# Kernel tuning notes

Hardware: AMD Instinct MI355X
Metric: run time of the kernel (lower is better)

## Reference

```python
import jax, jax.numpy as jnp
import numpy as np

L = 4          # dilation_depth
HID = 32       # hidden_channels
F_IN = 16
F_OUT = 16
K = 2          # conv kernel size


def setup_inputs() -> dict:
    key = jax.random.key(0)
    ks = jax.random.split(key, 20)
    B, T, N, F = 8, 512, 128, F_IN
    s = 0.1
    inp = {
        "X": jax.random.normal(ks[0], (B, T, N, F), jnp.float32),
        "A": jax.random.normal(ks[1], (N, N), jnp.float32) / jnp.sqrt(N).astype(jnp.float32),
        "in_w": jax.random.normal(ks[2], (F, 3 * HID), jnp.float32) * s,
        "in_b": jnp.zeros((3 * HID,), jnp.float32),
        "ct_w": jax.random.normal(ks[3], (L, K, HID, HID), jnp.float32) * s,
        "ct_b": jnp.zeros((L, HID), jnp.float32),
        "cs_w": jax.random.normal(ks[4], (L, K, HID, HID), jnp.float32) * s,
        "cs_b": jnp.zeros((L, HID), jnp.float32),
        "gcn_w": jax.random.normal(ks[5], (L, HID, HID), jnp.float32) * s,
        "gcn_b": jnp.zeros((L, HID), jnp.float32),
        "res_w": jax.random.normal(ks[6], (L, HID, HID), jnp.float32) * s,
        "res_b": jnp.zeros((L, HID), jnp.float32),
        "skip_w": jax.random.normal(ks[7], (L, HID, HID), jnp.float32) * s,
        "skip_b": jnp.zeros((L, HID), jnp.float32),
        "out1_w": jax.random.normal(ks[8], (HID, HID), jnp.float32) * s,
        "out1_b": jnp.zeros((HID,), jnp.float32),
        "out2_w": jax.random.normal(ks[9], (HID, F_OUT), jnp.float32) * s,
        "out2_b": jnp.zeros((F_OUT,), jnp.float32),
    }
    return inp


def _causal_conv(x, w, b, dilation):
    # x: [BN, T, C]; w: [K, C_in, C_out] (WIO); causal pad left by dilation*(K-1)
    pad = dilation * (w.shape[0] - 1)
    y = jax.lax.conv_general_dilated(
        x, w, window_strides=(1,), padding=[(pad, 0)],
        rhs_dilation=(dilation,), dimension_numbers=("NWC", "WIO", "NWC"))
    return y + b


def reference(X, A, in_w, in_b, ct_w, ct_b, cs_w, cs_b, gcn_w, gcn_b,
              res_w, res_b, skip_w, skip_b, out1_w, out1_b, out2_w, out2_b):
    B, T, N, F = X.shape
    Xp = X @ in_w + in_b                      # [B,T,N,3H]
    x_a, x_b, x_res = jnp.split(Xp, 3, axis=-1)
    H = x_a.shape[-1]
    # Faithful to source: raw reshape [B,T,N,H] -> [B*N,T,H] (no transpose), as in the original code.
    x_a_r = x_a.reshape(B * N, T, H)
    x_b_r = x_b.reshape(B * N, T, H)
    skip = jnp.zeros_like(x_res)
    for i in range(L):
        d = 2 ** i
        tcn = (jnp.tanh(_causal_conv(x_a_r, ct_w[i], ct_b[i], d))
               * jax.nn.sigmoid(_causal_conv(x_b_r, cs_w[i], cs_b[i], d)))
        tcn = tcn.reshape(B, N, T, H).transpose(0, 2, 1, 3)   # [B,T,N,H]
        gcn = jnp.einsum('ij,btjf->btif', A, x_res) @ gcn_w[i] + gcn_b[i]
        h = tcn + gcn
        x_res = (h @ res_w[i] + res_b[i]) + x_res
        skip = skip + (h @ skip_w[i] + skip_b[i])
    h = jax.nn.relu(skip)
    h = jax.nn.relu(h @ out1_w + out1_b)
    return h @ out2_w + out2_b
```

## Files before the change

kernel.cpp:

```cpp
#include <hip/hip_runtime.h>
#include <math.h>

#define T_ 512

typedef _Float16 half8 __attribute__((ext_vector_type(8)));
typedef _Float16 half4 __attribute__((ext_vector_type(4)));
typedef float f32x4 __attribute__((ext_vector_type(4)));

__device__ __forceinline__ float ts_act(float a, float b) {
    float e2a = __expf(a + a);
    float eb  = __expf(b);
    float num = (e2a - 1.0f) * eb;
    float den = (e2a + 1.0f) * (eb + 1.0f);
    return num * __builtin_amdgcn_rcpf(den);
}

__device__ __forceinline__ half4 pack4(f32x4 v) {
    half4 h;
    h[0] = (_Float16)v[0]; h[1] = (_Float16)v[1];
    h[2] = (_Float16)v[2]; h[3] = (_Float16)v[3];
    return h;
}

__global__ __launch_bounds__(256) void k_prep(
    const float* __restrict__ A,     const float* __restrict__ in_w,
    const float* __restrict__ in_b,
    const float* __restrict__ ct_w,  const float* __restrict__ ct_b,
    const float* __restrict__ cs_w,  const float* __restrict__ cs_b,
    const float* __restrict__ gcn_w, const float* __restrict__ res_w,
    const float* __restrict__ skip_w,
    const float* __restrict__ out1_w,const float* __restrict__ out2_w,
    _Float16* __restrict__ FR, float* __restrict__ BIAS)
{
    int idx = blockIdx.x * 256 + threadIdx.x;
    if (idx < 16384) {
        int j = idx & 7, L = (idx >> 3) & 63, tile = idx >> 9;
        int it = tile >> 2, kt = tile & 3;
        FR[idx] = (_Float16)A[(it * 16 + (L & 15)) * 128 + kt * 32 + (L >> 4) * 8 + j];
    } else if (idx < 24576) {
        int e = idx - 16384;
        int j = e & 7, L = (e >> 3) & 63, ct = (e >> 9) & 1, mat = e >> 10;
        int k = (L >> 4) * 8 + j, col = ct * 16 + (L & 15);
        int l = mat >> 1, br = mat & 1;
        const float* tw = (br ? cs_w : ct_w) + l * 2048;
        int bro = br * 32;
        float v = 0.f;
        if (k < 16) { for (int c = 0; c < 32; ++c) v += in_w[k*96 + bro + c] * tw[c*32 + col]; }
        else        { for (int c = 0; c < 32; ++c) v += in_w[(k-16)*96 + bro + c] * tw[1024 + c*32 + col]; }
        FR[idx] = (_Float16)v;
    } else if (idx < 39936) {
        int e = idx - 24576;
        int i = e & 3, L = (e >> 2) & 63, ct = (e >> 8) & 1, ks = (e >> 9) & 1, mat = e >> 10;
        int k = ks * 16 + (L >> 4) * 4 + i, col = ct * 16 + (L & 15);
        float v;
        if (mat < 12) {
            int l = mat / 3, r = mat - l * 3;
            const float* W = (r == 0) ? gcn_w : (r == 1) ? res_w : skip_w;
            v = W[l * 1024 + k * 32 + col];
        } else if (mat == 12) v = out1_w[k * 32 + col];
        else if (mat == 13)   v = (ct == 0) ? out2_w[k * 16 + (L & 15)] : 0.f;
        else                  v = (ks == 0) ? in_w[k * 96 + 64 + col] : 0.f;
        FR[idx] = (_Float16)v;
    } else if (idx < 40448) {
        int e = idx - 39936;
        int n = e & 31, br = (e >> 5) & 1, pvi = (e >> 6) & 1, l = e >> 7;
        const float* W  = br ? cs_w : ct_w;
        const float* bb = br ? cs_b : ct_b;
        int ibo = br * 32;
        float v = bb[l * 32 + n];
        for (int c = 0; c < 32; ++c) v += in_b[ibo + c] * W[l*2048 + 1024 + c*32 + n];
        if (pvi)
            for (int c = 0; c < 32; ++c) v += in_b[ibo + c] * W[l*2048 + c*32 + n];
        BIAS[e] = v;
    }
}

__global__ __launch_bounds__(256, 3) void k_fused(
    const float* __restrict__ X,
    const _Float16* __restrict__ FR,
    const float* __restrict__ BIAS,
    const float* __restrict__ in_b,
    const float* __restrict__ gcn_b,
    const float* __restrict__ res_b,
    const float* __restrict__ skip_b,
    const float* __restrict__ b1,
    const float* __restrict__ b2,
    float* __restrict__ out)
{
    __shared__ _Float16 Pld[128 * 88];
    __shared__ _Float16 xsT[2][32 * 136];

    const int bx = blockIdx.x;
    const int btid = ((bx & 7) << 9) | (bx >> 3);
    const int b = btid >> 9, t = btid & (T_ - 1);
    const int tid = threadIdx.x, lane = tid & 63, w = tid >> 6;
    const int lm = lane & 15, kb = lane >> 4;
    const int R = w * 32;
    const int row = lane >> 1, ch = lane & 1;

    const half8* AFv  = (const half8*)FR;
    const half8* W32v = (const half8*)(FR + 16384);
    const half4* W16v = (const half4*)(FR + 24576);
    const f32x4 zero4 = {0.f, 0.f, 0.f, 0.f};

    {
        const size_t nrow = (size_t)(b * 128 + R + row) * T_;
        const float4* xc = (const float4*)(X + (nrow + t) * 16 + ch * 8);
        float4 c0 = xc[0], c1 = xc[1];
        float4 p0[4], p1[4];
#pragma unroll
        for (int l = 0; l < 4; ++l) {
            const int d = 1 << l;
            if (t >= d) {
                const float4* xp = (const float4*)(X + (nrow + (t - d)) * 16 + ch * 8);
                p0[l] = xp[0]; p1[l] = xp[1];
            } else {
                p0[l] = make_float4(0.f, 0.f, 0.f, 0.f);
                p1[l] = make_float4(0.f, 0.f, 0.f, 0.f);
            }
        }
        half8 hv;
        hv[0]=(_Float16)c0.x; hv[1]=(_Float16)c0.y; hv[2]=(_Float16)c0.z; hv[3]=(_Float16)c0.w;
        hv[4]=(_Float16)c1.x; hv[5]=(_Float16)c1.y; hv[6]=(_Float16)c1.z; hv[7]=(_Float16)c1.w;
        *(half8*)&Pld[(R + row) * 88 + 64 + ch * 8] = hv;
#pragma unroll
        for (int l = 0; l < 4; ++l) {
            hv[0]=(_Float16)p0[l].x; hv[1]=(_Float16)p0[l].y; hv[2]=(_Float16)p0[l].z; hv[3]=(_Float16)p0[l].w;
            hv[4]=(_Float16)p1[l].x; hv[5]=(_Float16)p1[l].y; hv[6]=(_Float16)p1[l].z; hv[7]=(_Float16)p1[l].w;
            *(half8*)&Pld[(R + row) * 88 + l * 16 + ch * 8] = hv;
        }
    }

    f32x4 xm[2][2], skT[2][2];
    {
        const float4 x0 = *(const float4*)(X + ((size_t)btid * 128 + R + lm) * 16 + kb * 4);
        const float4 x1 = *(const float4*)(X + ((size_t)btid * 128 + R + 16 + lm) * 16 + kb * 4);
        half4 p0, p1;
        p0[0]=(_Float16)x0.x; p0[1]=(_Float16)x0.y; p0[2]=(_Float16)x0.z; p0[3]=(_Float16)x0.w;
        p1[0]=(_Float16)x1.x; p1[1]=(_Float16)x1.y; p1[2]=(_Float16)x1.z; p1[3]=(_Float16)x1.w;
#pragma unroll
        for (int f = 0; f < 2; ++f) {
            half4 wi = W16v[(56 + f) * 64 + lane];
            float bi = in_b[64 + f * 16 + lm];
            f32x4 cb; cb[0] = bi; cb[1] = bi; cb[2] = bi; cb[3] = bi;
            xm[0][f] = __builtin_amdgcn_mfma_f32_16x16x16f16(p0, wi, cb, 0, 0, 0);
            xm[1][f] = __builtin_amdgcn_mfma_f32_16x16x16f16(p1, wi, cb, 0, 0, 0);
        }
#pragma unroll
        for (int f3 = 0; f3 < 2; ++f3) {
            f32x4 s = zero4;
#pragma unroll
            for (int l = 0; l < 4; ++l) {
                const float4 q = *(const float4*)&skip_b[l * 32 + f3 * 16 + kb * 4];
                s[0] += q.x; s[1] += q.y; s[2] += q.z; s[3] += q.w;
            }
            skT[f3][0] = s; skT[f3][1] = s;
        }
    }

    const int fragoff = (kb < 2) ? kb * 8 : 64 + (kb - 2) * 8;
    const int lstep   = (kb < 2) ? 16 : 0;

#pragma unroll 1
    for (int l = 0; l < 4; ++l) {
        const bool pv = (t >= (1 << l));
        const float* B2 = BIAS + (l * 2 + (pv ? 1 : 0)) * 64;
        const int buf = l & 1;

#pragma unroll
        for (int mt = 0; mt < 2; ++mt)
#pragma unroll
            for (int f = 0; f < 2; ++f)
                *(half4*)&xsT[buf][(f * 16 + lm) * 136 + R + mt * 16 + kb * 4] = pack4(xm[mt][f]);

        half8 Afr[2][4];
#pragma unroll
        for (int mt = 0; mt < 2; ++mt)
#pragma unroll
            for (int kt = 0; kt < 4; ++kt)
                Afr[mt][kt] = AFv[((w * 2 + mt) * 4 + kt) * 64 + lane];
        const f32x4 cT0 = *(const f32x4*)&B2[0 * 16 + kb * 4];
        const f32x4 cT1 = *(const f32x4*)&B2[1 * 16 + kb * 4];
        const f32x4 cS0 = *(const f32x4*)&B2[32 + 0 * 16 + kb * 4];
        const f32x4 cS1 = *(const f32x4*)&B2[32 + 1 * 16 + kb * 4];

        __syncthreads();

        const int poff = fragoff + l * lstep;
        half8 pf0 = *(const half8*)&Pld[(R + lm) * 88 + poff];
        half8 pf1 = *(const half8*)&Pld[(R + 16 + lm) * 88 + poff];
        f32x4 dt[2][2], ds[2][2];
#pragma unroll
        for (int ct = 0; ct < 2; ++ct) {
            half8 wt = W32v[((l * 2 + 0) * 2 + ct) * 64 + lane];
            half8 ws = W32v[((l * 2 + 1) * 2 + ct) * 64 + lane];
            const f32x4 cT = ct ? cT1 : cT0;
            const f32x4 cS = ct ? cS1 : cS0;
            dt[ct][0] = __builtin_amdgcn_mfma_f32_16x16x32_f16(wt, pf0, cT, 0, 0, 0);
            dt[ct][1] = __builtin_amdgcn_mfma_f32_16x16x32_f16(wt, pf1, cT, 0, 0, 0);
            ds[ct][0] = __builtin_amdgcn_mfma_f32_16x16x32_f16(ws, pf0, cS, 0, 0, 0);
            ds[ct][1] = __builtin_amdgcn_mfma_f32_16x16x32_f16(ws, pf1, cS, 0, 0, 0);
        }

        f32x4 AxT[2][2];
#pragma unroll
        for (int f = 0; f < 2; ++f) {
            half8 xa[4];
#pragma unroll
            for (int kt = 0; kt < 4; ++kt)
                xa[kt] = *(const half8*)&xsT[buf][(f * 16 + lm) * 136 + kt * 32 + kb * 8];
#pragma unroll
            for (int mt = 0; mt < 2; ++mt) {
                f32x4 acc = zero4;
#pragma unroll
                for (int kt = 0; kt < 4; ++kt)
                    acc = __builtin_amdgcn_mfma_f32_16x16x32_f16(xa[kt], Afr[mt][kt], acc, 0, 0, 0);
                AxT[f][mt] = acc;
            }
        }

        f32x4 tcv[2][2];
#pragma unroll
        for (int ct = 0; ct < 2; ++ct)
#pragma unroll
            for (int mt = 0; mt < 2; ++mt)
#pragma unroll
                for (int r = 0; r < 4; ++r)
                    tcv[ct][mt][r] = ts_act(dt[ct][mt][r], ds[ct][mt][r]);

        half4 axh[2][2];
#pragma unroll
        for (int f = 0; f < 2; ++f)
#pragma unroll
            for (int mt = 0; mt < 2; ++mt) axh[f][mt] = pack4(AxT[f][mt]);
        half4 hh[2][2];
#pragma unroll
        for (int g = 0; g < 2; ++g) {
            half4 gw0 = W16v[((l * 3 + 0) * 4 + 0 + g) * 64 + lane];
            half4 gw1 = W16v[((l * 3 + 0) * 4 + 2 + g) * 64 + lane];
            const f32x4 gq = *(const f32x4*)&gcn_b[l * 32 + g * 16 + kb * 4];
#pragma unroll
            for (int mt = 0; mt < 2; ++mt) {
                f32x4 acc = __builtin_amdgcn_mfma_f32_16x16x16f16(gw0, axh[0][mt], gq, 0, 0, 0);
                acc = __builtin_amdgcn_mfma_f32_16x16x16f16(gw1, axh[1][mt], acc, 0, 0, 0);
#pragma unroll
                for (int r = 0; r < 4; ++r) acc[r] += tcv[g][mt][r];
                hh[g][mt] = pack4(acc);
            }
        }

#pragma unroll
        for (int mt = 0; mt < 2; ++mt)
#pragma unroll
            for (int f3 = 0; f3 < 2; ++f3) {
                half4 rw0 = W16v[((l * 3 + 1) * 4 + 0 + f3) * 64 + lane];
                half4 rw1 = W16v[((l * 3 + 1) * 4 + 2 + f3) * 64 + lane];
                f32x4 acc = __builtin_amdgcn_mfma_f32_16x16x16f16(hh[0][mt], rw0, xm[mt][f3], 0, 0, 0);
                xm[mt][f3] = __builtin_amdgcn_mfma_f32_16x16x16f16(hh[1][mt], rw1, acc, 0, 0, 0);
                float rb = res_b[l * 32 + f3 * 16 + lm];
#pragma unroll
                for (int r = 0; r < 4; ++r) xm[mt][f3][r] += rb;

                half4 sw0 = W16v[((l * 3 + 2) * 4 + 0 + f3) * 64 + lane];
                half4 sw1 = W16v[((l * 3 + 2) * 4 + 2 + f3) * 64 + lane];
                f32x4 acs = __builtin_amdgcn_mfma_f32_16x16x16f16(sw0, hh[0][mt], skT[f3][mt], 0, 0, 0);
                skT[f3][mt] = __builtin_amdgcn_mfma_f32_16x16x16f16(sw1, hh[1][mt], acs, 0, 0, 0);
            }
    }

    half4 rs[2][2];
#pragma unroll
    for (int g = 0; g < 2; ++g)
#pragma unroll
        for (int mt = 0; mt < 2; ++mt) {
            f32x4 v;
#pragma unroll
            for (int r = 0; r < 4; ++r) v[r] = fmaxf(skT[g][mt][r], 0.f);
            rs[g][mt] = pack4(v);
        }
    half4 h1h[2][2];
#pragma unroll
    for (int g4 = 0; g4 < 2; ++g4) {
        half4 w10 = W16v[(48 + 0 + g4) * 64 + lane];
        half4 w11 = W16v[(48 + 2 + g4) * 64 + lane];
        const f32x4 bq = *(const f32x4*)&b1[g4 * 16 + kb * 4];
#pragma unroll
        for (int mt = 0; mt < 2; ++mt) {
            f32x4 acc = __builtin_amdgcn_mfma_f32_16x16x16f16(w10, rs[0][mt], bq, 0, 0, 0);
            acc = __builtin_amdgcn_mfma_f32_16x16x16f16(w11, rs[1][mt], acc, 0, 0, 0);
            f32x4 v;
#pragma unroll
            for (int r = 0; r < 4; ++r) v[r] = fmaxf(acc[r], 0.f);
            h1h[g4][mt] = pack4(v);
        }
    }
    {
        half4 w20 = W16v[(52 + 0) * 64 + lane];
        half4 w21 = W16v[(52 + 2) * 64 + lane];
        const f32x4 b2q = *(const f32x4*)&b2[kb * 4];
#pragma unroll
        for (int mt = 0; mt < 2; ++mt) {
            f32x4 acc = __builtin_amdgcn_mfma_f32_16x16x16f16(w20, h1h[0][mt], b2q, 0, 0, 0);
            acc = __builtin_amdgcn_mfma_f32_16x16x16f16(w21, h1h[1][mt], acc, 0, 0, 0);
            float4 o = make_float4(acc[0], acc[1], acc[2], acc[3]);
            *(float4*)&out[((size_t)btid * 128 + R + mt * 16 + lm) * 16 + kb * 4] = o;
        }
    }
}

extern "C" void kernel_launch(void* const* d_in, const int* in_sizes, int n_in,
                              void* d_out, int out_size, void* d_ws, size_t ws_size,
                              hipStream_t stream)
{
    const float* X      = (const float*)d_in[0];
    const float* A      = (const float*)d_in[1];
    const float* in_w   = (const float*)d_in[2];
    const float* in_b   = (const float*)d_in[3];
    const float* ct_w   = (const float*)d_in[4];
    const float* ct_b   = (const float*)d_in[5];
    const float* cs_w   = (const float*)d_in[6];
    const float* cs_b   = (const float*)d_in[7];
    const float* gcn_w  = (const float*)d_in[8];
    const float* gcn_b  = (const float*)d_in[9];
    const float* res_w  = (const float*)d_in[10];
    const float* res_b  = (const float*)d_in[11];
    const float* skip_w = (const float*)d_in[12];
    const float* skip_b = (const float*)d_in[13];
    const float* out1_w = (const float*)d_in[14];
    const float* out1_b = (const float*)d_in[15];
    const float* out2_w = (const float*)d_in[16];
    const float* out2_b = (const float*)d_in[17];

    _Float16* FR   = (_Float16*)d_ws;
    float*    BIAS = (float*)((char*)d_ws + 79872);

    k_prep<<<158, 256, 0, stream>>>(A, in_w, in_b, ct_w, ct_b, cs_w, cs_b,
                                    gcn_w, res_w, skip_w, out1_w, out2_w,
                                    FR, BIAS);

    k_fused<<<8 * T_, 256, 0, stream>>>(X, FR, BIAS, in_b,
                                        gcn_b, res_b, skip_b,
                                        out1_b, out2_b, (float*)d_out);
}
```

Baseline: 195.6 us.

## Process two timesteps per block to share dilated-history X loads

Each block now handles two adjacent timesteps with 512 threads instead of one timestep with 256. The causal-conv history slabs (t-8,t-7,t-4..t+1) are loaded once into a shared Pld tile, so the overlapping past-timestep rows for the two timesteps are not fetched twice. This halves the grid and cuts redundant global loads of X, in exchange for more LDS per block, larger blocks and a stricter launch-bounds register budget that could cause spills or lower occupancy.

```diff
diff --git a/kernel.cpp b/kernel.cpp
--- a/kernel.cpp
+++ b/kernel.cpp
@@ -75,7 +75,7 @@
     }
 }
 
-__global__ __launch_bounds__(256, 3) void k_fused(
+__global__ __launch_bounds__(512, 4) void k_fused(
     const float* __restrict__ X,
     const _Float16* __restrict__ FR,
     const float* __restrict__ BIAS,
@@ -87,15 +87,17 @@
     const float* __restrict__ b2,
     float* __restrict__ out)
 {
-    __shared__ _Float16 Pld[128 * 88];
-    __shared__ _Float16 xsT[2][32 * 136];
+    __shared__ _Float16 Pld[128 * 136];
+    __shared__ _Float16 xsT[2][2][32 * 136];
 
     const int bx = blockIdx.x;
-    const int btid = ((bx & 7) << 9) | (bx >> 3);
-    const int b = btid >> 9, t = btid & (T_ - 1);
-    const int tid = threadIdx.x, lane = tid & 63, w = tid >> 6;
+    const int btp = ((bx & 7) << 8) | (bx >> 3);
+    const int b = btp >> 8, t0 = (btp & 255) * 2;
+    const int tid = threadIdx.x, lane = tid & 63;
+    const int g = tid >> 6, ts = g >> 2, ws = g & 3;
+    const int t = t0 + ts;
     const int lm = lane & 15, kb = lane >> 4;
-    const int R = w * 32;
+    const int R = ws * 32;
     const int row = lane >> 1, ch = lane & 1;
 
     const half8* AFv  = (const half8*)FR;
@@ -104,37 +106,28 @@
     const f32x4 zero4 = {0.f, 0.f, 0.f, 0.f};
 
     {
+        const int toff[8] = {-8, -7, -4, -3, -2, -1, 0, 1};
         const size_t nrow = (size_t)(b * 128 + R + row) * T_;
-        const float4* xc = (const float4*)(X + (nrow + t) * 16 + ch * 8);
-        float4 c0 = xc[0], c1 = xc[1];
-        float4 p0[4], p1[4];
-#pragma unroll
-        for (int l = 0; l < 4; ++l) {
-            const int d = 1 << l;
-            if (t >= d) {
-                const float4* xp = (const float4*)(X + (nrow + (t - d)) * 16 + ch * 8);
-                p0[l] = xp[0]; p1[l] = xp[1];
-            } else {
-                p0[l] = make_float4(0.f, 0.f, 0.f, 0.f);
-                p1[l] = make_float4(0.f, 0.f, 0.f, 0.f);
-            }
-        }
-        half8 hv;
-        hv[0]=(_Float16)c0.x; hv[1]=(_Float16)c0.y; hv[2]=(_Float16)c0.z; hv[3]=(_Float16)c0.w;
-        hv[4]=(_Float16)c1.x; hv[5]=(_Float16)c1.y; hv[6]=(_Float16)c1.z; hv[7]=(_Float16)c1.w;
-        *(half8*)&Pld[(R + row) * 88 + 64 + ch * 8] = hv;
-#pragma unroll
-        for (int l = 0; l < 4; ++l) {
-            hv[0]=(_Float16)p0[l].x; hv[1]=(_Float16)p0[l].y; hv[2]=(_Float16)p0[l].z; hv[3]=(_Float16)p0[l].w;
-            hv[4]=(_Float16)p1[l].x; hv[5]=(_Float16)p1[l].y; hv[6]=(_Float16)p1[l].z; hv[7]=(_Float16)p1[l].w;
-            *(half8*)&Pld[(R + row) * 88 + l * 16 + ch * 8] = hv;
+#pragma unroll
+        for (int sl = 0; sl < 4; ++sl) {
+            const int slab = ts * 4 + sl;
+            const int tt = t0 + toff[slab];
+            half8 hv = {0,0,0,0,0,0,0,0};
+            if (tt >= 0) {
+                const float4* xp = (const float4*)(X + (nrow + tt) * 16 + ch * 8);
+                float4 u0 = xp[0], u1 = xp[1];
+                hv[0]=(_Float16)u0.x; hv[1]=(_Float16)u0.y; hv[2]=(_Float16)u0.z; hv[3]=(_Float16)u0.w;
+                hv[4]=(_Float16)u1.x; hv[5]=(_Float16)u1.y; hv[6]=(_Float16)u1.z; hv[7]=(_Float16)u1.w;
+            }
+            *(half8*)&Pld[(R + row) * 136 + slab * 16 + ch * 8] = hv;
         }
     }
 
     f32x4 xm[2][2], skT[2][2];
     {
-        const float4 x0 = *(const float4*)(X + ((size_t)btid * 128 + R + lm) * 16 + kb * 4);
-        const float4 x1 = *(const float4*)(X + ((size_t)btid * 128 + R + 16 + lm) * 16 + kb * 4);
+        const size_t base = (size_t)(b * 512 + t) * 128;
+        const float4 x0 = *(const float4*)(X + (base + R + lm) * 16 + kb * 4);
+        const float4 x1 = *(const float4*)(X + (base + R + 16 + lm) * 16 + kb * 4);
         half4 p0, p1;
         p0[0]=(_Float16)x0.x; p0[1]=(_Float16)x0.y; p0[2]=(_Float16)x0.z; p0[3]=(_Float16)x0.w;
         p1[0]=(_Float16)x1.x; p1[1]=(_Float16)x1.y; p1[2]=(_Float16)x1.z; p1[3]=(_Float16)x1.w;
@@ -158,27 +151,25 @@
         }
     }
 
-    const int fragoff = (kb < 2) ? kb * 8 : 64 + (kb - 2) * 8;
-    const int lstep   = (kb < 2) ? 16 : 0;
-
 #pragma unroll 1
     for (int l = 0; l < 4; ++l) {
         const bool pv = (t >= (1 << l));
         const float* B2 = BIAS + (l * 2 + (pv ? 1 : 0)) * 64;
         const int buf = l & 1;
+        _Float16* xsb = (_Float16*)&xsT[ts][buf][0];
 
 #pragma unroll
         for (int mt = 0; mt < 2; ++mt)
 #pragma unroll
             for (int f = 0; f < 2; ++f)
-                *(half4*)&xsT[buf][(f * 16 + lm) * 136 + R + mt * 16 + kb * 4] = pack4(xm[mt][f]);
+                *(half4*)&xsb[(f * 16 + lm) * 136 + R + mt * 16 + kb * 4] = pack4(xm[mt][f]);
 
         half8 Afr[2][4];
 #pragma unroll
         for (int mt = 0; mt < 2; ++mt)
 #pragma unroll
             for (int kt = 0; kt < 4; ++kt)
-                Afr[mt][kt] = AFv[((w * 2 + mt) * 4 + kt) * 64 + lane];
+                Afr[mt][kt] = AFv[((ws * 2 + mt) * 4 + kt) * 64 + lane];
         const f32x4 cT0 = *(const f32x4*)&B2[0 * 16 + kb * 4];
         const f32x4 cT1 = *(const f32x4*)&B2[1 * 16 + kb * 4];
         const f32x4 cS0 = *(const f32x4*)&B2[32 + 0 * 16 + kb * 4];
@@ -186,20 +177,22 @@
 
         __syncthreads();
 
-        const int poff = fragoff + l * lstep;
-        half8 pf0 = *(const half8*)&Pld[(R + lm) * 88 + poff];
-        half8 pf1 = *(const half8*)&Pld[(R + 16 + lm) * 88 + poff];
+        const int pslab = ts + ((0x0245 >> (l << 2)) & 15);
+        const int cslab = 6 + ts;
+        const int poff = (kb < 2) ? pslab * 16 + kb * 8 : cslab * 16 + (kb - 2) * 8;
+        half8 pf0 = *(const half8*)&Pld[(R + lm) * 136 + poff];
+        half8 pf1 = *(const half8*)&Pld[(R + 16 + lm) * 136 + poff];
         f32x4 dt[2][2], ds[2][2];
 #pragma unroll
         for (int ct = 0; ct < 2; ++ct) {
             half8 wt = W32v[((l * 2 + 0) * 2 + ct) * 64 + lane];
-            half8 ws = W32v[((l * 2 + 1) * 2 + ct) * 64 + lane];
+            half8 ws8 = W32v[((l * 2 + 1) * 2 + ct) * 64 + lane];
             const f32x4 cT = ct ? cT1 : cT0;
             const f32x4 cS = ct ? cS1 : cS0;
             dt[ct][0] = __builtin_amdgcn_mfma_f32_16x16x32_f16(wt, pf0, cT, 0, 0, 0);
             dt[ct][1] = __builtin_amdgcn_mfma_f32_16x16x32_f16(wt, pf1, cT, 0, 0, 0);
-            ds[ct][0] = __builtin_amdgcn_mfma_f32_16x16x32_f16(ws, pf0, cS, 0, 0, 0);
-            ds[ct][1] = __builtin_amdgcn_mfma_f32_16x16x32_f16(ws, pf1, cS, 0, 0, 0);
+            ds[ct][0] = __builtin_amdgcn_mfma_f32_16x16x32_f16(ws8, pf0, cS, 0, 0, 0);
+            ds[ct][1] = __builtin_amdgcn_mfma_f32_16x16x32_f16(ws8, pf1, cS, 0, 0, 0);
         }
 
         f32x4 AxT[2][2];
@@ -208,7 +201,7 @@
             half8 xa[4];
 #pragma unroll
             for (int kt = 0; kt < 4; ++kt)
-                xa[kt] = *(const half8*)&xsT[buf][(f * 16 + lm) * 136 + kt * 32 + kb * 8];
+                xa[kt] = *(const half8*)&xsb[(f * 16 + lm) * 136 + kt * 32 + kb * 8];
 #pragma unroll
             for (int mt = 0; mt < 2; ++mt) {
                 f32x4 acc = zero4;
@@ -235,17 +228,17 @@
             for (int mt = 0; mt < 2; ++mt) axh[f][mt] = pack4(AxT[f][mt]);
         half4 hh[2][2];
 #pragma unroll
-        for (int g = 0; g < 2; ++g) {
-            half4 gw0 = W16v[((l * 3 + 0) * 4 + 0 + g) * 64 + lane];
-            half4 gw1 = W16v[((l * 3 + 0) * 4 + 2 + g) * 64 + lane];
-            const f32x4 gq = *(const f32x4*)&gcn_b[l * 32 + g * 16 + kb * 4];
+        for (int gg = 0; gg < 2; ++gg) {
+            half4 gw0 = W16v[((l * 3 + 0) * 4 + 0 + gg) * 64 + lane];
+            half4 gw1 = W16v[((l * 3 + 0) * 4 + 2 + gg) * 64 + lane];
+            const f32x4 gq = *(const f32x4*)&gcn_b[l * 32 + gg * 16 + kb * 4];
 #pragma unroll
             for (int mt = 0; mt < 2; ++mt) {
                 f32x4 acc = __builtin_amdgcn_mfma_f32_16x16x16f16(gw0, axh[0][mt], gq, 0, 0, 0);
                 acc = __builtin_amdgcn_mfma_f32_16x16x16f16(gw1, axh[1][mt], acc, 0, 0, 0);
 #pragma unroll
-                for (int r = 0; r < 4; ++r) acc[r] += tcv[g][mt][r];
-                hh[g][mt] = pack4(acc);
+                for (int r = 0; r < 4; ++r) acc[r] += tcv[gg][mt][r];
+                hh[gg][mt] = pack4(acc);
             }
         }
 
@@ -270,13 +263,13 @@
 
     half4 rs[2][2];
 #pragma unroll
-    for (int g = 0; g < 2; ++g)
+    for (int gg = 0; gg < 2; ++gg)
 #pragma unroll
         for (int mt = 0; mt < 2; ++mt) {
             f32x4 v;
 #pragma unroll
-            for (int r = 0; r < 4; ++r) v[r] = fmaxf(skT[g][mt][r], 0.f);
-            rs[g][mt] = pack4(v);
+            for (int r = 0; r < 4; ++r) v[r] = fmaxf(skT[gg][mt][r], 0.f);
+            rs[gg][mt] = pack4(v);
         }
     half4 h1h[2][2];
 #pragma unroll
@@ -298,12 +291,13 @@
         half4 w20 = W16v[(52 + 0) * 64 + lane];
         half4 w21 = W16v[(52 + 2) * 64 + lane];
         const f32x4 b2q = *(const f32x4*)&b2[kb * 4];
+        const size_t obase = (size_t)(b * 512 + t) * 128;
 #pragma unroll
         for (int mt = 0; mt < 2; ++mt) {
             f32x4 acc = __builtin_amdgcn_mfma_f32_16x16x16f16(w20, h1h[0][mt], b2q, 0, 0, 0);
             acc = __builtin_amdgcn_mfma_f32_16x16x16f16(w21, h1h[1][mt], acc, 0, 0, 0);
             float4 o = make_float4(acc[0], acc[1], acc[2], acc[3]);
-            *(float4*)&out[((size_t)btid * 128 + R + mt * 16 + lm) * 16 + kb * 4] = o;
+            *(float4*)&out[(obase + R + mt * 16 + lm) * 16 + kb * 4] = o;
         }
     }
 }
@@ -338,7 +332,7 @@
                                     gcn_w, res_w, skip_w, out1_w, out2_w,
                                     FR, BIAS);
 
-    k_fused<<<8 * T_, 256, 0, stream>>>(X, FR, BIAS, in_b,
-                                        gcn_b, res_b, skip_b,
-                                        out1_b, out2_b, (float*)d_out);
-}
+    k_fused<<<8 * (T_ / 2), 512, 0, stream>>>(X, FR, BIAS, in_b,
+                                              gcn_b, res_b, skip_b,
+                                              out1_b, out2_b, (float*)d_out);
+}
```

New measurement: 259.7 us. 32.8% more time.
